# Kernel tuning notes

Hardware: AMD Instinct MI355X
Metric: run time of the kernel (lower is better)

Reference implementation:

```python
import jax, jax.numpy as jnp
import numpy as np

N = 50000      # nodes per type
E = 262144     # edges per relation
D_IN = 256; D_OUT = 256; D_ATT = 64
NEG_SLOPE = 0.2


def setup_inputs() -> dict:
    key = jax.random.key(0)
    ks = jax.random.split(key, 22)
    rn = lambda k, s, sc=0.05: jax.random.normal(k, s, jnp.float32) * sc
    ri = lambda k, s: jax.random.randint(k, s, 0, N, jnp.int32)
    return {
        "hA": jax.random.normal(ks[0], (N, D_IN), jnp.float32),
        "hB": jax.random.normal(ks[1], (N, D_IN), jnp.float32),
        "Wself": rn(ks[2], (2, D_IN, D_OUT)),
        "bself": rn(ks[3], (2, D_OUT), 0.01),
        "Wq": rn(ks[4], (2, D_OUT, D_ATT)),
        "bq": rn(ks[5], (2, D_ATT), 0.01),
        "Wk": rn(ks[6], (2, D_OUT, D_ATT)),
        "bk": rn(ks[7], (2, D_ATT), 0.01),
        "Wal": rn(ks[8], (2, D_ATT)),
        "bal": rn(ks[9], (2,), 0.01),
        "War": rn(ks[10], (2, D_ATT)),
        "bar": rn(ks[11], (2,), 0.01),
        "Wsrc": rn(ks[12], (2, D_IN, D_OUT)),
        "bsrc": rn(ks[13], (2, D_OUT), 0.01),
        "Wdst": rn(ks[14], (2, D_IN, D_OUT)),
        "bdst": rn(ks[15], (2, D_OUT), 0.01),
        "attn_v": rn(ks[16], (2, D_OUT)),
        "gbias": rn(ks[17], (2, D_OUT), 0.01),
        "eab_src": ri(ks[18], (E,)),
        "eab_dst": ri(ks[19], (E,)),
        "eba_src": ri(ks[20], (E,)),
        "eba_dst": ri(ks[21], (E,)),
    }


def _gatv2(h_src, h_dst, src, dst, Ws, bs, Wd, bd, av, gb, n_dst):
    """DGL GATv2Conv, num_heads=1: e_uv = av . leaky_relu(fc_src(h)[u] + fc_dst(h)[v]),
    edge-softmax over incoming edges per dst, message = alpha * fc_src(h)[u], + bias."""
    ft_s = h_src @ Ws + bs                              # (Ns, D)
    ft_d = h_dst @ Wd + bd                              # (Nd, D)
    e = jax.nn.leaky_relu(ft_s[src] + ft_d[dst], NEG_SLOPE)  # (E, D)
    logits = e @ av                                     # (E,)
    m = jax.ops.segment_max(logits, dst, num_segments=n_dst)
    m = jnp.where(jnp.isfinite(m), m, 0.0)              # zero-in-degree safety
    ex = jnp.exp(logits - m[dst])
    den = jax.ops.segment_sum(ex, dst, num_segments=n_dst)
    alpha = ex / jnp.where(den[dst] > 0, den[dst], 1.0)  # (E,) edge softmax
    out = jax.ops.segment_sum(alpha[:, None] * ft_s[src], dst, num_segments=n_dst) + gb
    return out, alpha


def _forward(hA, hB, Wself, bself, Wq, bq, Wk, bk, Wal, bal, War, bar,
             Wsrc, bsrc, Wdst, bdst, attn_v, gbias,
             eab_src, eab_dst, eba_src, eba_dst):
    h = [hA, hB]
    z = [h[t] @ Wself[t] + bself[t] for t in range(2)]       # HeteroLinear W_self
    q = [z[t] @ Wq[t] + bq[t] for t in range(2)]
    k = [z[t] @ Wk[t] + bk[t] for t in range(2)]
    h_l = [k[t] @ Wal[t] + bal[t] for t in range(2)]          # (N,) = W_al(key)
    h_r = [q[t] @ War[t] + bar[t] for t in range(2)]          # (N,) = W_ar(query)
    att_self = [jax.nn.elu(h_l[t] + h_r[t]) for t in range(2)]

    # relation "ab": A -> B (etype index 0)
    rst_ab, a_ab = _gatv2(hA, hB, eab_src, eab_dst,
                          Wsrc[0], bsrc[0], Wdst[0], bdst[0], attn_v[0], gbias[0], N)
    eatt_b = jax.nn.elu((rst_ab @ Wk[1] + bk[1]) @ Wal[1] + bal[1] + h_r[1])
    # relation "ba": B -> A (etype index 1)
    rst_ba, a_ba = _gatv2(hB, hA, eba_src, eba_dst,
                          Wsrc[1], bsrc[1], Wdst[1], bdst[1], attn_v[1], gbias[1], N)
    eatt_a = jax.nn.elu((rst_ba @ Wk[0] + bk[0]) @ Wal[0] + bal[0] + h_r[0])

    attA = jax.nn.softmax(jnp.stack([att_self[0], eatt_a]), axis=0)  # (2, N)
    attB = jax.nn.softmax(jnp.stack([att_self[1], eatt_b]), axis=0)
    rstA = jax.nn.elu(attA[0][:, None] * z[0] + attA[1][:, None] * rst_ba)
    rstB = jax.nn.elu(attB[0][:, None] * z[1] + attB[1][:, None] * rst_ab)
    return jnp.stack([rstA, rstB])  # (2, N, D_OUT)


def reference(hA, hB, Wself, bself, Wq, bq, Wk, bk, Wal, bal, War, bar,
              Wsrc, bsrc, Wdst, bdst, attn_v, gbias,
              eab_src, eab_dst, eba_src, eba_dst):
    return _forward(hA, hB, Wself, bself, Wq, bq, Wk, bk, Wal, bal, War, bar,
                    Wsrc, bsrc, Wdst, bdst, attn_v, gbias,
                    eab_src, eab_dst, eba_src, eba_dst)
```

## Files before the change

### kernel.cpp

```cpp
#include <hip/hip_runtime.h>
#include <math.h>

#define NNODES 50000
#define NEDGES 262144
#define NEG_SLOPE 0.2f
#define NBINS (2 * NNODES)
#define NXP 391
#define NWG_GEMM (2 * NXP * 6)

typedef __attribute__((ext_vector_type(8))) short short8;
typedef __attribute__((ext_vector_type(4))) float f32x4;
typedef __attribute__((ext_vector_type(2))) float f32x2;
typedef __attribute__((ext_vector_type(4))) unsigned short u16x4;

#define AUX_PS 0
#define AUX_PD (2 * NNODES)
#define AUX_HL (4 * NNODES)
#define AUX_HR (6 * NNODES)

__device__ __forceinline__ float elu_f(float x) { return x > 0.f ? x : (__expf(x) - 1.f); }
__device__ __forceinline__ float bf2f(unsigned short u) {
    return __uint_as_float(((unsigned)u) << 16);
}
__device__ __forceinline__ f32x2 bfp2f(unsigned p) {
    f32x2 r;
    r.x = __uint_as_float(p << 16);
    r.y = __uint_as_float(p & 0xffff0000u);
    return r;
}
__device__ __forceinline__ unsigned short f2bf(float f) {
    unsigned u = __float_as_uint(f);
    unsigned r = (u + 0x7fffu + ((u >> 16) & 1u)) >> 16;
    return (unsigned short)r;
}

__global__ __launch_bounds__(256) void conv_bf16_2(const float* __restrict__ inA,
                                                   const float* __restrict__ inB,
                                                   unsigned short* __restrict__ outA,
                                                   unsigned short* __restrict__ outB,
                                                   int half) {
    int i = (blockIdx.x * 256 + threadIdx.x) * 4;
    if (i >= 2 * half) return;
    const float* in = (i < half) ? inA : inB;
    unsigned short* out = (i < half) ? outA : outB;
    int k = (i < half) ? i : i - half;
    float4 v = *reinterpret_cast<const float4*>(&in[k]);
    u16x4 o;
    o[0] = f2bf(v.x); o[1] = f2bf(v.y); o[2] = f2bf(v.z); o[3] = f2bf(v.w);
    *reinterpret_cast<u16x4*>(&out[k]) = o;
}

__global__ __launch_bounds__(256) void prep_all(
    const float* __restrict__ Wself, const float* __restrict__ Wsrc, const float* __restrict__ Wdst,
    const float* __restrict__ bself, const float* __restrict__ bsrc, const float* __restrict__ bdst,
    const float* __restrict__ Wq, const float* __restrict__ bq,
    const float* __restrict__ Wk, const float* __restrict__ bk,
    const float* __restrict__ Wal, const float* __restrict__ bal,
    const float* __restrict__ War, const float* __restrict__ bar,
    unsigned short* __restrict__ Wt, float* __restrict__ biasF,
    float* __restrict__ u_l, float* __restrict__ u_r,
    float* __restrict__ c_l, float* __restrict__ c_r) {
    if (blockIdx.x < 2) {
        int t = blockIdx.x;
        int d = threadIdx.x;
        float sl = 0.f, sr = 0.f;
        for (int j = 0; j < 64; ++j) {
            sl += Wk[((size_t)t * 256 + d) * 64 + j] * Wal[t * 64 + j];
            sr += Wq[((size_t)t * 256 + d) * 64 + j] * War[t * 64 + j];
        }
        u_l[t * 256 + d] = sl;
        u_r[t * 256 + d] = sr;
        if (d == 0) {
            float cl = bal[t], cr = bar[t];
            for (int j = 0; j < 64; ++j) {
                cl += bk[t * 64 + j] * Wal[t * 64 + j];
                cr += bq[t * 64 + j] * War[t * 64 + j];
            }
            c_l[t] = cl; c_r[t] = cr;
        }
        return;
    }
    int r = blockIdx.x - 2;
    int t = r / 768;
    int n = r % 768;
    int seg = n >> 8;
    int nn = n & 255;
    const float* W; const float* bv; int ti;
    if (seg == 0)      { W = Wself; bv = bself; ti = t; }
    else if (seg == 1) { W = Wsrc;  bv = bsrc;  ti = t; }
    else               { W = Wdst;  bv = bdst;  ti = 1 - t; }
    int k = threadIdx.x;
    float val = W[(size_t)ti * 65536 + (size_t)k * 256 + nn];
    Wt[(size_t)r * 256 + k] = f2bf(val);
    if (k == 0) biasF[r] = bv[ti * 256 + nn];
}

__global__ __launch_bounds__(256) void hist2(const int* __restrict__ dab,
                                             const int* __restrict__ dba,
                                             int* __restrict__ counts) {
    int e = blockIdx.x * 256 + threadIdx.x;
    if (e < NEDGES) atomicAdd(&counts[dab[e]], 1);
    else if (e < 2 * NEDGES) atomicAdd(&counts[NNODES + dba[e - NEDGES]], 1);
}

__global__ __launch_bounds__(256) void scan1v(const int* __restrict__ counts,
                                              int* __restrict__ incl,
                                              int* __restrict__ bsum, int n) {
    __shared__ int s[256];
    int t = threadIdx.x;
    int base = blockIdx.x * 1024 + t * 4;
    int4 v = make_int4(0, 0, 0, 0);
    if (base < n) v = *reinterpret_cast<const int4*>(&counts[base]);
    int l0 = v.x, l1 = l0 + v.y, l2 = l1 + v.z, l3 = l2 + v.w;
    s[t] = l3;
    __syncthreads();
#pragma unroll
    for (int off = 1; off < 256; off <<= 1) {
        int x = (t >= off) ? s[t - off] : 0;
        __syncthreads();
        s[t] += x;
        __syncthreads();
    }
    int ex = s[t] - l3;
    if (base < n)
        *reinterpret_cast<int4*>(&incl[base]) = make_int4(ex + l0, ex + l1, ex + l2, ex + l3);
    if (t == 255) bsum[blockIdx.x] = s[255];
}

__global__ __launch_bounds__(512) void scan2(int* __restrict__ bsum, int nb) {
    __shared__ int s[512];
    int t = threadIdx.x;
    s[t] = (t < nb) ? bsum[t] : 0;
    __syncthreads();
#pragma unroll
    for (int off = 1; off < 512; off <<= 1) {
        int x = (t >= off) ? s[t - off] : 0;
        __syncthreads();
        s[t] += x;
        __syncthreads();
    }
    if (t < nb) bsum[t] = s[t];
}

__global__ __launch_bounds__(256) void scan3v(const int* __restrict__ counts,
                                              int* __restrict__ incl_to_rs,
                                              const int* __restrict__ bsum,
                                              int* __restrict__ cursor, int n, int nb) {
    int base = blockIdx.x * 1024 + threadIdx.x * 4;
    if (blockIdx.x == 0 && threadIdx.x == 0) incl_to_rs[n] = bsum[nb - 1];
    if (base >= n) return;
    int bofs = (blockIdx.x > 0) ? bsum[blockIdx.x - 1] : 0;
    int4 ic = *reinterpret_cast<const int4*>(&incl_to_rs[base]);
    int4 cn = *reinterpret_cast<const int4*>(&counts[base]);
    int4 st = make_int4(bofs + ic.x - cn.x, bofs + ic.y - cn.y,
                        bofs + ic.z - cn.z, bofs + ic.w - cn.w);
    *reinterpret_cast<int4*>(&incl_to_rs[base]) = st;
    *reinterpret_cast<int4*>(&cursor[base]) = st;
}

__global__ __launch_bounds__(256) void scatter2(const int* __restrict__ sab,
                                                const int* __restrict__ dab,
                                                const int* __restrict__ sba,
                                                const int* __restrict__ dba,
                                                int* __restrict__ cursor,
                                                int* __restrict__ sorted_src) {
    int e = blockIdx.x * 256 + threadIdx.x;
    if (e < NEDGES) {
        int pos = atomicAdd(&cursor[dab[e]], 1);
        sorted_src[pos] = sab[e];
    } else if (e < 2 * NEDGES) {
        int k = e - NEDGES;
        int pos = atomicAdd(&cursor[NNODES + dba[k]], 1);
        sorted_src[pos] = sba[k];
    }
}

__global__ __launch_bounds__(256, 4) void gemm_mfma(
    const unsigned short* __restrict__ hAb,
    const unsigned short* __restrict__ hBb,
    const unsigned short* __restrict__ Wt,
    const float* __restrict__ biasF,
    const float* __restrict__ attn_v,
    const float* __restrict__ u_l,
    const float* __restrict__ u_r,
    unsigned short* __restrict__ bufA,
    unsigned short* __restrict__ bufB,
    float* __restrict__ aux,
    int M)
{
    __shared__ unsigned short lds[16384];
    const int tid = threadIdx.x;
    const int lane = tid & 63;
    const int w = tid >> 6;
    const int wm = w >> 1, wn = w & 1;

    const int nwg = NWG_GEMM;
    const int q = nwg / 8, r = nwg % 8;
    int orig = blockIdx.x;
    int xcd = orig % 8, idx = orig / 8;
    int wgid = (xcd < r) ? (xcd * (q + 1) + idx) : (r * (q + 1) + (xcd - r) * q + idx);
    int t   = wgid / (NXP * 6);
    int rem = wgid % (NXP * 6);
    int xp  = rem / 6;
    int yc  = rem % 6;

    const int row0 = xp * 128;
    const int col0 = yc * 128;
    const unsigned short* Ain = t ? hBb : hAb;
    const unsigned short* Wtt = Wt + (size_t)t * 768 * 256;
    const float* bias = biasF + t * 768;
    unsigned short* Cout = t ? bufB : bufA;

    f32x4 acc[4][4] = {};

    const unsigned short* gA[2];
    const unsigned short* gB[2];
#pragma unroll
    for (int rr = 0; rr < 2; ++rr) {
        int qq = rr * 256 + tid;
        int row = qq >> 2;
        int c = (qq & 3) ^ ((row >> 1) & 3);
        int ga = min(row0 + row, M - 1);
        gA[rr] = Ain + (size_t)ga * 256 + c * 8;
        gB[rr] = Wtt + (size_t)(col0 + row) * 256 + c * 8;
    }

#define STAGE(buf, kt)                                                                   \
    {                                                                                    \
        unsigned short* Ad = lds + (buf) * 4096;                                         \
        unsigned short* Bd = lds + 8192 + (buf) * 4096;                                  \
        _Pragma("unroll")                                                                \
        for (int rr = 0; rr < 2; ++rr) {                                                 \
            __builtin_amdgcn_global_load_lds(                                            \
                (const __attribute__((address_space(1))) unsigned int*)(gA[rr] + (kt)),  \
                (__attribute__((address_space(3))) unsigned int*)(Ad + ((rr * 256 + w * 64) << 3)), \
                16, 0, 0);                                                               \
            __builtin_amdgcn_global_load_lds(                                            \
                (const __attribute__((address_space(1))) unsigned int*)(gB[rr] + (kt)),  \
                (__attribute__((address_space(3))) unsigned int*)(Bd + ((rr * 256 + w * 64) << 3)), \
                16, 0, 0);                                                               \
        }                                                                                \
    }

    STAGE(0, 0);
    STAGE(1, 32);

#pragma unroll
    for (int it = 0; it < 8; ++it) {
        const int cur = it & 1;
        if (it < 7) { asm volatile("s_waitcnt vmcnt(4)" ::: "memory"); }
        else        { asm volatile("s_waitcnt vmcnt(0)" ::: "memory"); }
        __builtin_amdgcn_s_barrier();
        __builtin_amdgcn_sched_barrier(0);

        const unsigned short* As = lds + cur * 4096;
        const unsigned short* Bs = lds + 8192 + cur * 4096;
        short8 a[4], b[4];
#pragma unroll
        for (int i = 0; i < 4; ++i) {
            int ar = wm * 64 + i * 16 + (lane & 15);
            a[i] = *reinterpret_cast<const short8*>(
                &As[ar * 32 + (((lane >> 4) ^ ((ar >> 1) & 3)) << 3)]);
            int br = wn * 64 + i * 16 + (lane & 15);
            b[i] = *reinterpret_cast<const short8*>(
                &Bs[br * 32 + (((lane >> 4) ^ ((br >> 1) & 3)) << 3)]);
        }
#pragma unroll
        for (int i = 0; i < 4; ++i)
#pragma unroll
            for (int j = 0; j < 4; ++j)
                acc[i][j] = __builtin_amdgcn_mfma_f32_16x16x32_bf16(a[i], b[j], acc[i][j], 0, 0, 0);

        asm volatile("s_waitcnt lgkmcnt(0)" ::: "memory");
        __builtin_amdgcn_sched_barrier(0);
        __builtin_amdgcn_s_barrier();
        if (it < 6) STAGE(cur, (it + 2) * 32);
    }
#undef STAGE

#pragma unroll
    for (int j = 0; j < 4; ++j) {
        int colg = wn * 4 + j;
        int ci = lane & 15;
        float bv = bias[col0 + colg * 16 + ci];
#pragma unroll
        for (int i = 0; i < 4; ++i) {
            int rowb = wm * 64 + i * 16 + ((lane >> 4) << 2);
#pragma unroll
            for (int v = 0; v < 4; ++v) {
                int row = rowb + v;
                int g2 = colg ^ ((row >> 2) & 3);
                lds[row * 128 + g2 * 16 + ci] = f2bf(acc[i][j][v] + bv);
            }
        }
    }
    __syncthreads();

    const int seg = yc >> 1;
    const float* avp1; float* axp1;
    const float* avp2 = nullptr; float* axp2 = nullptr;
    if (seg == 0) {
        avp1 = u_l + t * 256;            axp1 = aux + AUX_HL + (size_t)t * NNODES;
        avp2 = u_r + t * 256;            axp2 = aux + AUX_HR + (size_t)t * NNODES;
    } else if (seg == 1) {
        avp1 = attn_v + t * 256;         axp1 = aux + AUX_PS + (size_t)t * NNODES;
    } else {
        avp1 = attn_v + (1 - t) * 256;   axp1 = aux + AUX_PD + (size_t)(1 - t) * NNODES;
    }

#pragma unroll
    for (int p = 0; p < 8; ++p) {
        int idx = p * 256 + tid;
        int row = idx >> 4;
        int ch = idx & 15;
        int g2 = (ch >> 1) ^ ((row >> 2) & 3);
        int grow = row0 + row;
        bool ok = grow < M;
        short8 val = *reinterpret_cast<const short8*>(&lds[row * 128 + g2 * 16 + ((ch & 1) << 3)]);
        if (ok)
            *reinterpret_cast<short8*>(&Cout[(size_t)grow * 768 + col0 + ch * 8]) = val;
        int colb = (yc & 1) * 128 + ch * 8;
        float4 w0v = *reinterpret_cast<const float4*>(&avp1[colb]);
        float4 w1v = *reinterpret_cast<const float4*>(&avp1[colb + 4]);
        float p1 = w0v.x * bf2f((unsigned short)val[0]) + w0v.y * bf2f((unsigned short)val[1])
                 + w0v.z * bf2f((unsigned short)val[2]) + w0v.w * bf2f((unsigned short)val[3])
                 + w1v.x * bf2f((unsigned short)val[4]) + w1v.y * bf2f((unsigned short)val[5])
                 + w1v.z * bf2f((unsigned short)val[6]) + w1v.w * bf2f((unsigned short)val[7]);
        p1 += __shfl_xor(p1, 1);
        p1 += __shfl_xor(p1, 2);
        p1 += __shfl_xor(p1, 4);
        p1 += __shfl_xor(p1, 8);
        if ((tid & 15) == 0 && ok) atomicAdd(&axp1[grow], p1);
        if (avp2) {
            float4 y0 = *reinterpret_cast<const float4*>(&avp2[colb]);
            float4 y1 = *reinterpret_cast<const float4*>(&avp2[colb + 4]);
            float p2 = y0.x * bf2f((unsigned short)val[0]) + y0.y * bf2f((unsigned short)val[1])
                     + y0.z * bf2f((unsigned short)val[2]) + y0.w * bf2f((unsigned short)val[3])
                     + y1.x * bf2f((unsigned short)val[4]) + y1.y * bf2f((unsigned short)val[5])
                     + y1.z * bf2f((unsigned short)val[6]) + y1.w * bf2f((unsigned short)val[7]);
            p2 += __shfl_xor(p2, 1);
            p2 += __shfl_xor(p2, 2);
            p2 += __shfl_xor(p2, 4);
            p2 += __shfl_xor(p2, 8);
            if ((tid & 15) == 0 && ok) atomicAdd(&axp2[grow], p2);
        }
    }
}

__global__ __launch_bounds__(256) void gat_fused(
    const unsigned short* __restrict__ bufA, const unsigned short* __restrict__ bufB,
    const int* __restrict__ sorted_src, const int* __restrict__ row_start,
    const float* __restrict__ attn_v, const float* __restrict__ gbias,
    const float* __restrict__ u_l,
    const float* __restrict__ c_l, const float* __restrict__ c_r,
    const float* __restrict__ aux,
    float* __restrict__ out)
{
    const int tid = threadIdx.x;
    const int l = tid & 15;
    const int gBase = tid & 48;
    const int nd = blockIdx.x * 16 + (tid >> 4);
    if (nd >= 2 * NNODES) return;
    const int rel = nd >= NNODES;
    const int d = nd - rel * NNODES;
    const int td = rel ? 0 : 1;

    const unsigned short* zbuf = td ? bufB : bufA;
    const unsigned short* ftS = (rel ? bufB : bufA) + 256;
    const unsigned short* ftD = zbuf + 512;
    const float clv = c_l[td], crv = c_r[td];

    f32x2 fd2[8], av2[8];
    {
        const unsigned short* fdp = &ftD[(size_t)d * 768 + l * 16];
        uint4 d0 = *reinterpret_cast<const uint4*>(fdp);
        uint4 d1 = *reinterpret_cast<const uint4*>(fdp + 8);
        fd2[0] = bfp2f(d0.x); fd2[1] = bfp2f(d0.y); fd2[2] = bfp2f(d0.z); fd2[3] = bfp2f(d0.w);
        fd2[4] = bfp2f(d1.x); fd2[5] = bfp2f(d1.y); fd2[6] = bfp2f(d1.z); fd2[7] = bfp2f(d1.w);
        const float* avp = attn_v + rel * 256 + l * 16;
#pragma unroll
        for (int e = 0; e < 4; ++e) {
            float4 a = *reinterpret_cast<const float4*>(&avp[e * 4]);
            av2[2 * e].x = a.x; av2[2 * e].y = a.y;
            av2[2 * e + 1].x = a.z; av2[2 * e + 1].y = a.w;
        }
    }

    const float pd6 = 0.6f * aux[AUX_PD + (size_t)rel * NNODES + d];
    const float hlv = aux[AUX_HL + (size_t)td * NNODES + d] + clv;
    const float hrv = aux[AUX_HR + (size_t)td * NNODES + d] + crv;
    const float a0 = elu_f(hlv + hrv);
    const float* psb = aux + AUX_PS + (size_t)rel * NNODES;

    const int p0  = row_start[nd];
    const int cnt = row_start[nd + 1] - p0;
    float den = 0.f;
    f32x2 acc2[8];
#pragma unroll
    for (int e = 0; e < 8; ++e) { acc2[e].x = 0.f; acc2[e].y = 0.f; }

#define PROC2(X0, X1, QX, Y0, Y1, QY)                                            \
    {                                                                            \
        f32x2 fa2[8], fb2[8];                                                    \
        fa2[0] = bfp2f((X0).x); fa2[1] = bfp2f((X0).y);                          \
        fa2[2] = bfp2f((X0).z); fa2[3] = bfp2f((X0).w);                          \
        fa2[4] = bfp2f((X1).x); fa2[5] = bfp2f((X1).y);                          \
        fa2[6] = bfp2f((X1).z); fa2[7] = bfp2f((X1).w);                          \
        fb2[0] = bfp2f((Y0).x); fb2[1] = bfp2f((Y0).y);                          \
        fb2[2] = bfp2f((Y0).z); fb2[3] = bfp2f((Y0).w);                          \
        fb2[4] = bfp2f((Y1).x); fb2[5] = bfp2f((Y1).y);                          \
        fb2[6] = bfp2f((Y1).z); fb2[7] = bfp2f((Y1).w);                          \
        float Sa = 0.f, Sb = 0.f;                                                \
        _Pragma("unroll")                                                        \
        for (int e = 0; e < 8; ++e) {                                            \
            f32x2 xa = fa2[e] + fd2[e];                                          \
            f32x2 xb = fb2[e] + fd2[e];                                          \
            Sa += av2[e].x * fabsf(xa.x);                                        \
            Sa += av2[e].y * fabsf(xa.y);                                        \
            Sb += av2[e].x * fabsf(xb.x);                                        \
            Sb += av2[e].y * fabsf(xb.y);                                        \
        }                                                                        \
        Sa += __shfl_xor(Sa, 1); Sb += __shfl_xor(Sb, 1);                        \
        Sa += __shfl_xor(Sa, 2); Sb += __shfl_xor(Sb, 2);                        \
        Sa += __shfl_xor(Sa, 4); Sb += __shfl_xor(Sb, 4);                        \
        Sa += __shfl_xor(Sa, 8); Sb += __shfl_xor(Sb, 8);                        \
        float wa = __expf(fmaf(0.6f, (QX), pd6) + 0.4f * Sa);                    \
        float wb = __expf(fmaf(0.6f, (QY), pd6) + 0.4f * Sb);                    \
        den += wa + wb;                                                          \
        _Pragma("unroll")                                                        \
        for (int e = 0; e < 8; ++e) acc2[e] += wa * fa2[e] + wb * fb2[e];        \
    }

    for (int base = 0; base < cnt; base += 16) {
        int nloc = min(16, cnt - base);
        int sv = 0; float psl = 0.f;
        if (base + l < cnt) { sv = sorted_src[p0 + base + l]; psl = psb[sv]; }
        int j = 0;
        for (; j + 4 <= nloc; j += 4) {
            int s0 = __shfl(sv, gBase + j);
            int s1 = __shfl(sv, gBase + j + 1);
            int s2 = __shfl(sv, gBase + j + 2);
            int s3 = __shfl(sv, gBase + j + 3);
            float q0 = __shfl(psl, gBase + j);
            float q1 = __shfl(psl, gBase + j + 1);
            float q2 = __shfl(psl, gBase + j + 2);
            float q3 = __shfl(psl, gBase + j + 3);
            const unsigned short* rp0 = &ftS[(size_t)s0 * 768 + l * 16];
            const unsigned short* rp1 = &ftS[(size_t)s1 * 768 + l * 16];
            const unsigned short* rp2 = &ftS[(size_t)s2 * 768 + l * 16];
            const unsigned short* rp3 = &ftS[(size_t)s3 * 768 + l * 16];
            uint4 A0 = *reinterpret_cast<const uint4*>(rp0);
            uint4 A1 = *reinterpret_cast<const uint4*>(rp0 + 8);
            uint4 B0 = *reinterpret_cast<const uint4*>(rp1);
            uint4 B1 = *reinterpret_cast<const uint4*>(rp1 + 8);
            uint4 C0 = *reinterpret_cast<const uint4*>(rp2);
            uint4 C1 = *reinterpret_cast<const uint4*>(rp2 + 8);
            uint4 D0 = *reinterpret_cast<const uint4*>(rp3);
            uint4 D1 = *reinterpret_cast<const uint4*>(rp3 + 8);
            PROC2(A0, A1, q0, B0, B1, q1);
            PROC2(C0, C1, q2, D0, D1, q3);
        }
        for (; j + 2 <= nloc; j += 2) {
            int s0 = __shfl(sv, gBase + j);
            int s1 = __shfl(sv, gBase + j + 1);
            float q0 = __shfl(psl, gBase + j);
            float q1 = __shfl(psl, gBase + j + 1);
            const unsigned short* rp0 = &ftS[(size_t)s0 * 768 + l * 16];
            const unsigned short* rp1 = &ftS[(size_t)s1 * 768 + l * 16];
            uint4 A0 = *reinterpret_cast<const uint4*>(rp0);
            uint4 A1 = *reinterpret_cast<const uint4*>(rp0 + 8);
            uint4 B0 = *reinterpret_cast<const uint4*>(rp1);
            uint4 B1 = *reinterpret_cast<const uint4*>(rp1 + 8);
            PROC2(A0, A1, q0, B0, B1, q1);
        }
        if (j < nloc) {
            int s0 = __shfl(sv, gBase + j);
            float q0 = __shfl(psl, gBase + j);
            const unsigned short* rp0 = &ftS[(size_t)s0 * 768 + l * 16];
            uint4 A0 = *reinterpret_cast<const uint4*>(rp0);
            uint4 A1 = *reinterpret_cast<const uint4*>(rp0 + 8);
            f32x2 fa2[8];
            fa2[0] = bfp2f(A0.x); fa2[1] = bfp2f(A0.y); fa2[2] = bfp2f(A0.z); fa2[3] = bfp2f(A0.w);
            fa2[4] = bfp2f(A1.x); fa2[5] = bfp2f(A1.y); fa2[6] = bfp2f(A1.z); fa2[7] = bfp2f(A1.w);
            float Sa = 0.f;
#pragma unroll
            for (int e = 0; e < 8; ++e) {
                f32x2 xa = fa2[e] + fd2[e];
                Sa += av2[e].x * fabsf(xa.x);
                Sa += av2[e].y * fabsf(xa.y);
            }
            Sa += __shfl_xor(Sa, 1);
            Sa += __shfl_xor(Sa, 2);
            Sa += __shfl_xor(Sa, 4);
            Sa += __shfl_xor(Sa, 8);
            float wa = __expf(fmaf(0.6f, q0, pd6) + 0.4f * Sa);
            den += wa;
#pragma unroll
            for (int e = 0; e < 8; ++e) acc2[e] += wa * fa2[e];
        }
    }
#undef PROC2

    float inv = den > 0.f ? 1.f / den : 1.f;
    const float* gb = gbias + rel * 256 + l * 16;
    const float* ulp = u_l + td * 256 + l * 16;
    f32x2 v2[8];
    float dotv = 0.f;
#pragma unroll
    for (int e = 0; e < 4; ++e) {
        float4 g = *reinterpret_cast<const float4*>(&gb[e * 4]);
        float4 u = *reinterpret_cast<const float4*>(&ulp[e * 4]);
        v2[2 * e].x     = acc2[2 * e].x     * inv + g.x;
        v2[2 * e].y     = acc2[2 * e].y     * inv + g.y;
        v2[2 * e + 1].x = acc2[2 * e + 1].x * inv + g.z;
        v2[2 * e + 1].y = acc2[2 * e + 1].y * inv + g.w;
        dotv += v2[2 * e].x * u.x + v2[2 * e].y * u.y
              + v2[2 * e + 1].x * u.z + v2[2 * e + 1].y * u.w;
    }
    dotv += __shfl_xor(dotv, 1);
    dotv += __shfl_xor(dotv, 2);
    dotv += __shfl_xor(dotv, 4);
    dotv += __shfl_xor(dotv, 8);
    const float ea = elu_f(dotv + clv + hrv);

    float mx = fmaxf(a0, ea);
    float e0 = __expf(a0 - mx), e1 = __expf(ea - mx);
    float is = 1.f / (e0 + e1);
    float w0 = e0 * is, w1 = e1 * is;

    const unsigned short* zrow = zbuf + (size_t)d * 768 + l * 16;
    uint4 z0 = *reinterpret_cast<const uint4*>(zrow);
    uint4 z1 = *reinterpret_cast<const uint4*>(zrow + 8);
    f32x2 zf2[8];
    zf2[0] = bfp2f(z0.x); zf2[1] = bfp2f(z0.y); zf2[2] = bfp2f(z0.z); zf2[3] = bfp2f(z0.w);
    zf2[4] = bfp2f(z1.x); zf2[5] = bfp2f(z1.y); zf2[6] = bfp2f(z1.z); zf2[7] = bfp2f(z1.w);

    float* orow = out + ((size_t)(1 - rel) * NNODES + d) * 256 + l * 16;
#pragma unroll
    for (int e = 0; e < 4; ++e) {
        float4 o;
        o.x = elu_f(w0 * zf2[2 * e].x     + w1 * v2[2 * e].x);
        o.y = elu_f(w0 * zf2[2 * e].y     + w1 * v2[2 * e].y);
        o.z = elu_f(w0 * zf2[2 * e + 1].x + w1 * v2[2 * e + 1].x);
        o.w = elu_f(w0 * zf2[2 * e + 1].y + w1 * v2[2 * e + 1].y);
        *reinterpret_cast<float4*>(&orow[e * 4]) = o;
    }
}

extern "C" void kernel_launch(void* const* d_in, const int* in_sizes, int n_in,
                              void* d_out, int out_size, void* d_ws, size_t ws_size,
                              hipStream_t stream) {
    const float* hA     = (const float*)d_in[0];
    const float* hB     = (const float*)d_in[1];
    const float* Wself  = (const float*)d_in[2];
    const float* bself  = (const float*)d_in[3];
    const float* Wq     = (const float*)d_in[4];
    const float* bq     = (const float*)d_in[5];
    const float* Wk     = (const float*)d_in[6];
    const float* bk     = (const float*)d_in[7];
    const float* Wal    = (const float*)d_in[8];
    const float* bal    = (const float*)d_in[9];
    const float* War    = (const float*)d_in[10];
    const float* bar    = (const float*)d_in[11];
    const float* Wsrc   = (const float*)d_in[12];
    const float* bsrc   = (const float*)d_in[13];
    const float* Wdst   = (const float*)d_in[14];
    const float* bdst   = (const float*)d_in[15];
    const float* attn_v = (const float*)d_in[16];
    const float* gbias  = (const float*)d_in[17];
    const int* eab_src  = (const int*)d_in[18];
    const int* eab_dst  = (const int*)d_in[19];
    const int* eba_src  = (const int*)d_in[20];
    const int* eba_dst  = (const int*)d_in[21];
    float* out = (float*)d_out;
    char* ws = (char*)d_ws;

    const size_t SZ_BUF = (size_t)NNODES * 768 * sizeof(unsigned short);
    const size_t SZ_H   = (size_t)NNODES * 256 * sizeof(unsigned short);
    size_t off = 0;
    auto alloc = [&](size_t bytes) { void* p = ws + off; off = (off + bytes + 255) & ~(size_t)255; return p; };
    unsigned short* bufA = (unsigned short*)alloc(SZ_BUF);
    unsigned short* bufB = (unsigned short*)alloc(SZ_BUF);
    unsigned short* hAb  = (unsigned short*)alloc(SZ_H);
    unsigned short* hBb  = (unsigned short*)alloc(SZ_H);
    unsigned short* Wt   = (unsigned short*)alloc(2 * 768 * 256 * sizeof(unsigned short));
    float* biasF   = (float*)alloc(2 * 768 * sizeof(float));
    float* aux     = (float*)alloc((size_t)8 * NNODES * sizeof(float));
    int* counts    = (int*)alloc(NBINS * sizeof(int));
    int* row_start = (int*)alloc((NBINS + 4) * sizeof(int));
    int* cursor    = (int*)alloc(NBINS * sizeof(int));
    int* bsum      = (int*)alloc(512 * sizeof(int));
    int* sorted_src= (int*)alloc(2 * (size_t)NEDGES * sizeof(int));
    float* u_l     = (float*)alloc(2 * 256 * sizeof(float));
    float* u_r     = (float*)alloc(2 * 256 * sizeof(float));
    float* c_l     = (float*)alloc(2 * sizeof(float));
    float* c_r     = (float*)alloc(2 * sizeof(float));

    hipMemsetAsync(counts, 0, NBINS * sizeof(int), stream);
    hipMemsetAsync(aux, 0, (size_t)8 * NNODES * sizeof(float), stream);

    const int HN = NNODES * 256;
    conv_bf16_2<<<(2 * HN / 4 + 255) / 256, 256, 0, stream>>>(hA, hB, hAb, hBb, HN);
    prep_all<<<2 + 2 * 768, 256, 0, stream>>>(Wself, Wsrc, Wdst, bself, bsrc, bdst,
                                              Wq, bq, Wk, bk, Wal, bal, War, bar,
                                              Wt, biasF, u_l, u_r, c_l, c_r);

    const int e2blocks = (2 * NEDGES + 255) / 256;
    hist2<<<e2blocks, 256, 0, stream>>>(eab_dst, eba_dst, counts);
    const int sblocks = (NBINS + 1023) / 1024;
    scan1v<<<sblocks, 256, 0, stream>>>(counts, row_start, bsum, NBINS);
    scan2<<<1, 512, 0, stream>>>(bsum, sblocks);
    scan3v<<<sblocks, 256, 0, stream>>>(counts, row_start, bsum, cursor, NBINS, sblocks);
    scatter2<<<e2blocks, 256, 0, stream>>>(eab_src, eab_dst, eba_src, eba_dst, cursor, sorted_src);

    gemm_mfma<<<NWG_GEMM, 256, 0, stream>>>(hAb, hBb, Wt, biasF, attn_v, u_l, u_r,
                                            bufA, bufB, aux, NNODES);

    gat_fused<<<(2 * NNODES + 15) / 16, 256, 0, stream>>>(bufA, bufB, sorted_src, row_start,
                                                          attn_v, gbias, u_l,
                                                          c_l, c_r, aux, out);
}
```

Measured before the change: 272.6 us.

## Fuse prep kernels, merge scan stages, and degree-sort node order for GAT

The bf16 conversion, destination histogram and weight prep are fused into one launch. The second and third scan stages are merged, and the two memsets become one. Scan1 also builds a histogram of node in-degrees, and a new pass uses it to order nodes by descending degree. gat_fused then processes nodes in that order, so wavefronts get nodes with similar edge counts and less load imbalance. The cost is an extra indirection and weaker memory locality for per-node rows, since node order inside each degree bucket follows atomic order.

```diff
diff --git a/kernel.cpp b/kernel.cpp
--- a/kernel.cpp
+++ b/kernel.cpp
@@ -8,6 +8,10 @@
 #define NXP 391
 #define NWG_GEMM (2 * NXP * 6)
 
+#define CONV_B 25000
+#define HIST_B 2048
+#define PREP_B 1538
+
 typedef __attribute__((ext_vector_type(8))) short short8;
 typedef __attribute__((ext_vector_type(4))) float f32x4;
 typedef __attribute__((ext_vector_type(2))) float f32x2;
@@ -34,23 +38,10 @@
     return (unsigned short)r;
 }
 
-__global__ __launch_bounds__(256) void conv_bf16_2(const float* __restrict__ inA,
-                                                   const float* __restrict__ inB,
-                                                   unsigned short* __restrict__ outA,
-                                                   unsigned short* __restrict__ outB,
-                                                   int half) {
-    int i = (blockIdx.x * 256 + threadIdx.x) * 4;
-    if (i >= 2 * half) return;
-    const float* in = (i < half) ? inA : inB;
-    unsigned short* out = (i < half) ? outA : outB;
-    int k = (i < half) ? i : i - half;
-    float4 v = *reinterpret_cast<const float4*>(&in[k]);
-    u16x4 o;
-    o[0] = f2bf(v.x); o[1] = f2bf(v.y); o[2] = f2bf(v.z); o[3] = f2bf(v.w);
-    *reinterpret_cast<u16x4*>(&out[k]) = o;
-}
-
-__global__ __launch_bounds__(256) void prep_all(
+__global__ __launch_bounds__(256) void fused_prep(
+    const float* __restrict__ hA, const float* __restrict__ hB,
+    unsigned short* __restrict__ hAb, unsigned short* __restrict__ hBb, int half,
+    const int* __restrict__ dab, const int* __restrict__ dba, int* __restrict__ counts,
     const float* __restrict__ Wself, const float* __restrict__ Wsrc, const float* __restrict__ Wdst,
     const float* __restrict__ bself, const float* __restrict__ bsrc, const float* __restrict__ bdst,
     const float* __restrict__ Wq, const float* __restrict__ bq,
@@ -59,9 +50,30 @@
     const float* __restrict__ War, const float* __restrict__ bar,
     unsigned short* __restrict__ Wt, float* __restrict__ biasF,
     float* __restrict__ u_l, float* __restrict__ u_r,
-    float* __restrict__ c_l, float* __restrict__ c_r) {
-    if (blockIdx.x < 2) {
-        int t = blockIdx.x;
+    float* __restrict__ c_l, float* __restrict__ c_r)
+{
+    int b = blockIdx.x;
+    if (b < CONV_B) {
+        int i = (b * 256 + threadIdx.x) * 4;
+        if (i >= 2 * half) return;
+        const float* in = (i < half) ? hA : hB;
+        unsigned short* out = (i < half) ? hAb : hBb;
+        int k = (i < half) ? i : i - half;
+        float4 v = *reinterpret_cast<const float4*>(&in[k]);
+        u16x4 o;
+        o[0] = f2bf(v.x); o[1] = f2bf(v.y); o[2] = f2bf(v.z); o[3] = f2bf(v.w);
+        *reinterpret_cast<u16x4*>(&out[k]) = o;
+        return;
+    }
+    if (b < CONV_B + HIST_B) {
+        int e = (b - CONV_B) * 256 + threadIdx.x;
+        if (e < NEDGES) atomicAdd(&counts[dab[e]], 1);
+        else atomicAdd(&counts[NNODES + dba[e - NEDGES]], 1);
+        return;
+    }
+    int pb = b - CONV_B - HIST_B;
+    if (pb < 2) {
+        int t = pb;
         int d = threadIdx.x;
         float sl = 0.f, sr = 0.f;
         for (int j = 0; j < 64; ++j) {
@@ -80,7 +92,7 @@
         }
         return;
     }
-    int r = blockIdx.x - 2;
+    int r = pb - 2;
     int t = r / 768;
     int n = r % 768;
     int seg = n >> 8;
@@ -95,25 +107,26 @@
     if (k == 0) biasF[r] = bv[ti * 256 + nn];
 }
 
-__global__ __launch_bounds__(256) void hist2(const int* __restrict__ dab,
-                                             const int* __restrict__ dba,
-                                             int* __restrict__ counts) {
-    int e = blockIdx.x * 256 + threadIdx.x;
-    if (e < NEDGES) atomicAdd(&counts[dab[e]], 1);
-    else if (e < 2 * NEDGES) atomicAdd(&counts[NNODES + dba[e - NEDGES]], 1);
-}
-
 __global__ __launch_bounds__(256) void scan1v(const int* __restrict__ counts,
                                               int* __restrict__ incl,
-                                              int* __restrict__ bsum, int n) {
+                                              int* __restrict__ bsum,
+                                              int* __restrict__ deghist, int n) {
     __shared__ int s[256];
+    __shared__ int dh[64];
     int t = threadIdx.x;
+    if (t < 64) dh[t] = 0;
     int base = blockIdx.x * 1024 + t * 4;
     int4 v = make_int4(0, 0, 0, 0);
     if (base < n) v = *reinterpret_cast<const int4*>(&counts[base]);
     int l0 = v.x, l1 = l0 + v.y, l2 = l1 + v.z, l3 = l2 + v.w;
     s[t] = l3;
     __syncthreads();
+    if (base < n) {
+        atomicAdd(&dh[min(v.x, 63)], 1);
+        atomicAdd(&dh[min(v.y, 63)], 1);
+        atomicAdd(&dh[min(v.z, 63)], 1);
+        atomicAdd(&dh[min(v.w, 63)], 1);
+    }
 #pragma unroll
     for (int off = 1; off < 256; off <<= 1) {
         int x = (t >= off) ? s[t - off] : 0;
@@ -125,31 +138,37 @@
     if (base < n)
         *reinterpret_cast<int4*>(&incl[base]) = make_int4(ex + l0, ex + l1, ex + l2, ex + l3);
     if (t == 255) bsum[blockIdx.x] = s[255];
-}
-
-__global__ __launch_bounds__(512) void scan2(int* __restrict__ bsum, int nb) {
-    __shared__ int s[512];
+    __syncthreads();
+    if (t < 64 && dh[t]) atomicAdd(&deghist[t], dh[t]);
+}
+
+__global__ __launch_bounds__(256) void scan23v(const int* __restrict__ counts,
+                                               int* __restrict__ incl_to_rs,
+                                               const int* __restrict__ bsum,
+                                               int* __restrict__ cursor,
+                                               const int* __restrict__ deghist,
+                                               int* __restrict__ degcur,
+                                               int n, int nb) {
+    __shared__ int s[128];
     int t = threadIdx.x;
-    s[t] = (t < nb) ? bsum[t] : 0;
+    if (t < 128) s[t] = (t < nb) ? bsum[t] : 0;
     __syncthreads();
 #pragma unroll
-    for (int off = 1; off < 512; off <<= 1) {
-        int x = (t >= off) ? s[t - off] : 0;
+    for (int off = 1; off < 128; off <<= 1) {
+        int x = 0;
+        if (t < 128 && t >= off) x = s[t - off];
         __syncthreads();
-        s[t] += x;
+        if (t < 128) s[t] += x;
         __syncthreads();
     }
-    if (t < nb) bsum[t] = s[t];
-}
-
-__global__ __launch_bounds__(256) void scan3v(const int* __restrict__ counts,
-                                              int* __restrict__ incl_to_rs,
-                                              const int* __restrict__ bsum,
-                                              int* __restrict__ cursor, int n, int nb) {
-    int base = blockIdx.x * 1024 + threadIdx.x * 4;
-    if (blockIdx.x == 0 && threadIdx.x == 0) incl_to_rs[n] = bsum[nb - 1];
+    if (blockIdx.x == 0 && t == 0) {
+        incl_to_rs[n] = s[nb - 1];
+        int off = 0;
+        for (int b2 = 63; b2 >= 0; --b2) { degcur[b2] = off; off += deghist[b2]; }
+    }
+    int base = blockIdx.x * 1024 + t * 4;
     if (base >= n) return;
-    int bofs = (blockIdx.x > 0) ? bsum[blockIdx.x - 1] : 0;
+    int bofs = (blockIdx.x > 0) ? s[blockIdx.x - 1] : 0;
     int4 ic = *reinterpret_cast<const int4*>(&incl_to_rs[base]);
     int4 cn = *reinterpret_cast<const int4*>(&counts[base]);
     int4 st = make_int4(bofs + ic.x - cn.x, bofs + ic.y - cn.y,
@@ -158,21 +177,33 @@
     *reinterpret_cast<int4*>(&cursor[base]) = st;
 }
 
-__global__ __launch_bounds__(256) void scatter2(const int* __restrict__ sab,
-                                                const int* __restrict__ dab,
-                                                const int* __restrict__ sba,
-                                                const int* __restrict__ dba,
-                                                int* __restrict__ cursor,
-                                                int* __restrict__ sorted_src) {
-    int e = blockIdx.x * 256 + threadIdx.x;
-    if (e < NEDGES) {
-        int pos = atomicAdd(&cursor[dab[e]], 1);
-        sorted_src[pos] = sab[e];
-    } else if (e < 2 * NEDGES) {
-        int k = e - NEDGES;
-        int pos = atomicAdd(&cursor[NNODES + dba[k]], 1);
-        sorted_src[pos] = sba[k];
-    }
+__global__ __launch_bounds__(256) void scatter2n(const int* __restrict__ sab,
+                                                 const int* __restrict__ dab,
+                                                 const int* __restrict__ sba,
+                                                 const int* __restrict__ dba,
+                                                 int* __restrict__ cursor,
+                                                 int* __restrict__ sorted_src,
+                                                 const int* __restrict__ row_start,
+                                                 int* __restrict__ degcur,
+                                                 int* __restrict__ node_order) {
+    int b = blockIdx.x;
+    if (b < HIST_B) {
+        int e = b * 256 + threadIdx.x;
+        if (e < NEDGES) {
+            int pos = atomicAdd(&cursor[dab[e]], 1);
+            sorted_src[pos] = sab[e];
+        } else {
+            int k = e - NEDGES;
+            int pos = atomicAdd(&cursor[NNODES + dba[k]], 1);
+            sorted_src[pos] = sba[k];
+        }
+        return;
+    }
+    int idx = (b - HIST_B) * 256 + threadIdx.x;
+    if (idx >= NBINS) return;
+    int cnt = row_start[idx + 1] - row_start[idx];
+    int pos = atomicAdd(&degcur[min(cnt, 63)], 1);
+    node_order[pos] = idx;
 }
 
 __global__ __launch_bounds__(256, 4) void gemm_mfma(
@@ -350,6 +381,7 @@
 __global__ __launch_bounds__(256) void gat_fused(
     const unsigned short* __restrict__ bufA, const unsigned short* __restrict__ bufB,
     const int* __restrict__ sorted_src, const int* __restrict__ row_start,
+    const int* __restrict__ node_order,
     const float* __restrict__ attn_v, const float* __restrict__ gbias,
     const float* __restrict__ u_l,
     const float* __restrict__ c_l, const float* __restrict__ c_r,
@@ -359,8 +391,9 @@
     const int tid = threadIdx.x;
     const int l = tid & 15;
     const int gBase = tid & 48;
-    const int nd = blockIdx.x * 16 + (tid >> 4);
-    if (nd >= 2 * NNODES) return;
+    const int nd0 = blockIdx.x * 16 + (tid >> 4);
+    if (nd0 >= 2 * NNODES) return;
+    const int nd = node_order[nd0];
     const int rel = nd >= NNODES;
     const int d = nd - rel * NNODES;
     const int td = rel ? 0 : 1;
@@ -587,36 +620,41 @@
     float* biasF   = (float*)alloc(2 * 768 * sizeof(float));
     float* aux     = (float*)alloc((size_t)8 * NNODES * sizeof(float));
     int* counts    = (int*)alloc(NBINS * sizeof(int));
+    int* deghist   = (int*)alloc(64 * sizeof(int));
+    size_t zspan   = (char*)(deghist + 64) - (char*)aux;
     int* row_start = (int*)alloc((NBINS + 4) * sizeof(int));
     int* cursor    = (int*)alloc(NBINS * sizeof(int));
     int* bsum      = (int*)alloc(512 * sizeof(int));
+    int* degcur    = (int*)alloc(64 * sizeof(int));
+    int* node_order= (int*)alloc(NBINS * sizeof(int));
     int* sorted_src= (int*)alloc(2 * (size_t)NEDGES * sizeof(int));
     float* u_l     = (float*)alloc(2 * 256 * sizeof(float));
     float* u_r     = (float*)alloc(2 * 256 * sizeof(float));
     float* c_l     = (float*)alloc(2 * sizeof(float));
     float* c_r     = (float*)alloc(2 * sizeof(float));
 
-    hipMemsetAsync(counts, 0, NBINS * sizeof(int), stream);
-    hipMemsetAsync(aux, 0, (size_t)8 * NNODES * sizeof(float), stream);
+    hipMemsetAsync(aux, 0, zspan, stream);
 
     const int HN = NNODES * 256;
-    conv_bf16_2<<<(2 * HN / 4 + 255) / 256, 256, 0, stream>>>(hA, hB, hAb, hBb, HN);
-    prep_all<<<2 + 2 * 768, 256, 0, stream>>>(Wself, Wsrc, Wdst, bself, bsrc, bdst,
-                                              Wq, bq, Wk, bk, Wal, bal, War, bar,
-                                              Wt, biasF, u_l, u_r, c_l, c_r);
-
-    const int e2blocks = (2 * NEDGES + 255) / 256;
-    hist2<<<e2blocks, 256, 0, stream>>>(eab_dst, eba_dst, counts);
+    fused_prep<<<CONV_B + HIST_B + PREP_B, 256, 0, stream>>>(
+        hA, hB, hAb, hBb, HN,
+        eab_dst, eba_dst, counts,
+        Wself, Wsrc, Wdst, bself, bsrc, bdst,
+        Wq, bq, Wk, bk, Wal, bal, War, bar,
+        Wt, biasF, u_l, u_r, c_l, c_r);
+
     const int sblocks = (NBINS + 1023) / 1024;
-    scan1v<<<sblocks, 256, 0, stream>>>(counts, row_start, bsum, NBINS);
-    scan2<<<1, 512, 0, stream>>>(bsum, sblocks);
-    scan3v<<<sblocks, 256, 0, stream>>>(counts, row_start, bsum, cursor, NBINS, sblocks);
-    scatter2<<<e2blocks, 256, 0, stream>>>(eab_src, eab_dst, eba_src, eba_dst, cursor, sorted_src);
+    scan1v<<<sblocks, 256, 0, stream>>>(counts, row_start, bsum, deghist, NBINS);
+    scan23v<<<sblocks, 256, 0, stream>>>(counts, row_start, bsum, cursor,
+                                         deghist, degcur, NBINS, sblocks);
+    scatter2n<<<HIST_B + (NBINS + 255) / 256, 256, 0, stream>>>(
+        eab_src, eab_dst, eba_src, eba_dst, cursor, sorted_src,
+        row_start, degcur, node_order);
 
     gemm_mfma<<<NWG_GEMM, 256, 0, stream>>>(hAb, hBb, Wt, biasF, attn_v, u_l, u_r,
                                             bufA, bufB, aux, NNODES);
 
     gat_fused<<<(2 * NNODES + 15) / 16, 256, 0, stream>>>(bufA, bufB, sorted_src, row_start,
-                                                          attn_v, gbias, u_l,
+                                                          node_order, attn_v, gbias, u_l,
                                                           c_l, c_r, aux, out);
 }
```

Result: slower. 643.1 us (+135.9%).
